# Kernel optimization log

Hardware: AMD Instinct MI355X
Metric: run time of the kernel (lower is better)

The kernel has to match this reference:

```python
import jax, jax.numpy as jnp
import numpy as np

NODES = 8192
RANK = 10  # hardcoded inner dim in the original module


def setup_inputs() -> dict:
    key = jax.random.key(0)
    k1, k2 = jax.random.split(key)
    nodevec1 = jax.random.normal(k1, (NODES, RANK), dtype=jnp.float32)
    nodevec2 = jax.random.normal(k2, (RANK, NODES), dtype=jnp.float32)
    return {"nodevec1": nodevec1, "nodevec2": nodevec2}


def reference(nodevec1, nodevec2):
    # [N, 10] @ [10, N] -> [N, N]; relu; row softmax (dim=1)
    scores = jax.nn.relu(jnp.matmul(nodevec1, nodevec2))
    return jax.nn.softmax(scores, axis=1)
```

## Files before the change

kernel.cpp:

```cpp
#include <hip/hip_runtime.h>


#define NODES 8192
#define RANK  10

#define K1_TPB   1024
#define K1_NWAVE (K1_TPB / 64)
#define K1_RPB   32
#define K1_NBLK  (NODES / K1_RPB)
#define K1_CHUNK 8

__global__ __launch_bounds__(K1_TPB)
void rowsum_kernel(const float* __restrict__ nv1,
                   const float* __restrict__ nv2,
                   float* __restrict__ rowinv)
{
    const int t    = threadIdx.x;
    const int lane = t & 63;
    const int wave = t >> 6;
    const int row0 = blockIdx.x * K1_RPB;

    float4 b[2][RANK];
#pragma unroll
    for (int g = 0; g < 2; ++g) {
        const int j = g * 4096 + t * 4;
#pragma unroll
        for (int k = 0; k < RANK; ++k)
            b[g][k] = *reinterpret_cast<const float4*>(nv2 + k * NODES + j);
    }

    __shared__ float red[K1_NWAVE][K1_RPB];

    for (int c = 0; c < K1_RPB; c += K1_CHUNK) {
        float psum[K1_CHUNK];
#pragma unroll
        for (int r = 0; r < K1_CHUNK; ++r) {
            const int row = row0 + c + r;
            float a[RANK];
#pragma unroll
            for (int k = 0; k < RANK; ++k) a[k] = nv1[row * RANK + k];

            float sum = 0.0f;
#pragma unroll
            for (int g = 0; g < 2; ++g) {
                float4 acc = make_float4(0.f, 0.f, 0.f, 0.f);
#pragma unroll
                for (int k = 0; k < RANK; ++k) {
                    acc.x = fmaf(a[k], b[g][k].x, acc.x);
                    acc.y = fmaf(a[k], b[g][k].y, acc.y);
                    acc.z = fmaf(a[k], b[g][k].z, acc.z);
                    acc.w = fmaf(a[k], b[g][k].w, acc.w);
                }
                sum += __expf(fmaxf(acc.x, 0.f)) + __expf(fmaxf(acc.y, 0.f))
                     + __expf(fmaxf(acc.z, 0.f)) + __expf(fmaxf(acc.w, 0.f));
            }
            psum[r] = sum;
        }
#pragma unroll
        for (int r = 0; r < K1_CHUNK; ++r) {
#pragma unroll
            for (int m = 32; m >= 1; m >>= 1)
                psum[r] += __shfl_xor(psum[r], m, 64);
        }
        if (lane == 0) {
#pragma unroll
            for (int r = 0; r < K1_CHUNK; ++r) red[wave][c + r] = psum[r];
        }
    }

    __syncthreads();
    if (t < K1_RPB) {
        float s = 0.0f;
#pragma unroll
        for (int w = 0; w < K1_NWAVE; ++w) s += red[w][t];
        rowinv[row0 + t] = 1.0f / s;
    }
}

#define K2_TPB  256
#define K2_RPB  8
#define K2_SEGS (NODES / (K2_TPB * 4))
#define K2_NBLK ((NODES / K2_RPB) * K2_SEGS)

__global__ __launch_bounds__(K2_TPB, 8)
void stream_kernel(const float* __restrict__ nv1,
                   const float* __restrict__ nv2,
                   const float* __restrict__ rowinv,
                   float* __restrict__ out)
{
    const int t      = threadIdx.x;
    const int seg    = blockIdx.x & (K2_SEGS - 1);
    const int rowblk = blockIdx.x >> 3;
    const int row0   = rowblk * K2_RPB;
    const int j      = seg * (K2_TPB * 4) + t * 4;

    float4 b[RANK];
#pragma unroll
    for (int k = 0; k < RANK; ++k)
        b[k] = *reinterpret_cast<const float4*>(nv2 + k * NODES + j);

#pragma unroll 2
    for (int r = 0; r < K2_RPB; ++r) {
        const int row = row0 + r;
        const float inv = rowinv[row];
        float a[RANK];
#pragma unroll
        for (int k = 0; k < RANK; ++k) a[k] = nv1[row * RANK + k];

        float4 acc = make_float4(0.f, 0.f, 0.f, 0.f);
#pragma unroll
        for (int k = 0; k < RANK; ++k) {
            acc.x = fmaf(a[k], b[k].x, acc.x);
            acc.y = fmaf(a[k], b[k].y, acc.y);
            acc.z = fmaf(a[k], b[k].z, acc.z);
            acc.w = fmaf(a[k], b[k].w, acc.w);
        }
        float4 o;
        o.x = __expf(fmaxf(acc.x, 0.f)) * inv;
        o.y = __expf(fmaxf(acc.y, 0.f)) * inv;
        o.z = __expf(fmaxf(acc.z, 0.f)) * inv;
        o.w = __expf(fmaxf(acc.w, 0.f)) * inv;
        *reinterpret_cast<float4*>(out + (size_t)row * NODES + j) = o;
    }
}

extern "C" void kernel_launch(void* const* d_in, const int* in_sizes, int n_in,
                              void* d_out, int out_size, void* d_ws, size_t ws_size,
                              hipStream_t stream)
{
    const float* nv1 = (const float*)d_in[0];
    const float* nv2 = (const float*)d_in[1];
    float* out    = (float*)d_out;
    float* rowinv = (float*)d_ws;

    rowsum_kernel<<<K1_NBLK, K1_TPB, 0, stream>>>(nv1, nv2, rowinv);
    stream_kernel<<<K2_NBLK, K2_TPB, 0, stream>>>(nv1, nv2, rowinv, out);
}
```

Before: 288.1 us.

## Fold log2e into B, use exp2 with log-sum offset, persistent stream grid

```diff
diff --git a/kernel.cpp b/kernel.cpp
--- a/kernel.cpp
+++ b/kernel.cpp
@@ -3,6 +3,7 @@
 
 #define NODES 8192
 #define RANK  10
+#define L2E   1.4426950408889634f
 
 #define K1_TPB   1024
 #define K1_NWAVE (K1_TPB / 64)
@@ -13,7 +14,7 @@
 __global__ __launch_bounds__(K1_TPB)
 void rowsum_kernel(const float* __restrict__ nv1,
                    const float* __restrict__ nv2,
-                   float* __restrict__ rowinv)
+                   float* __restrict__ rowsum)
 {
     const int t    = threadIdx.x;
     const int lane = t & 63;
@@ -25,8 +26,11 @@
     for (int g = 0; g < 2; ++g) {
         const int j = g * 4096 + t * 4;
 #pragma unroll
-        for (int k = 0; k < RANK; ++k)
-            b[g][k] = *reinterpret_cast<const float4*>(nv2 + k * NODES + j);
+        for (int k = 0; k < RANK; ++k) {
+            float4 v = *reinterpret_cast<const float4*>(nv2 + k * NODES + j);
+            v.x *= L2E; v.y *= L2E; v.z *= L2E; v.w *= L2E;
+            b[g][k] = v;
+        }
     }
 
     __shared__ float red[K1_NWAVE][K1_RPB];
@@ -51,8 +55,10 @@
                     acc.z = fmaf(a[k], b[g][k].z, acc.z);
                     acc.w = fmaf(a[k], b[g][k].w, acc.w);
                 }
-                sum += __expf(fmaxf(acc.x, 0.f)) + __expf(fmaxf(acc.y, 0.f))
-                     + __expf(fmaxf(acc.z, 0.f)) + __expf(fmaxf(acc.w, 0.f));
+                sum += __builtin_amdgcn_exp2f(fmaxf(acc.x, 0.f))
+                     + __builtin_amdgcn_exp2f(fmaxf(acc.y, 0.f))
+                     + __builtin_amdgcn_exp2f(fmaxf(acc.z, 0.f))
+                     + __builtin_amdgcn_exp2f(fmaxf(acc.w, 0.f));
             }
             psum[r] = sum;
         }
@@ -73,54 +79,62 @@
         float s = 0.0f;
 #pragma unroll
         for (int w = 0; w < K1_NWAVE; ++w) s += red[w][t];
-        rowinv[row0 + t] = 1.0f / s;
+        rowsum[row0 + t] = s;
     }
 }
 
-#define K2_TPB  256
-#define K2_RPB  8
-#define K2_SEGS (NODES / (K2_TPB * 4))
-#define K2_NBLK ((NODES / K2_RPB) * K2_SEGS)
+#define K2_TPB   256
+#define K2_RPB   8
+#define K2_SEGW  (K2_TPB * 4)
+#define K2_NSEG  (NODES / K2_SEGW)
+#define K2_GRID  2048
+#define K2_RSTR  (K2_GRID / K2_NSEG)
+#define K2_ITERS (NODES / K2_RPB / K2_RSTR)
 
 __global__ __launch_bounds__(K2_TPB, 8)
 void stream_kernel(const float* __restrict__ nv1,
                    const float* __restrict__ nv2,
-                   const float* __restrict__ rowinv,
+                   const float* __restrict__ rowsum,
                    float* __restrict__ out)
 {
-    const int t      = threadIdx.x;
-    const int seg    = blockIdx.x & (K2_SEGS - 1);
-    const int rowblk = blockIdx.x >> 3;
-    const int row0   = rowblk * K2_RPB;
-    const int j      = seg * (K2_TPB * 4) + t * 4;
+    const int t     = threadIdx.x;
+    const int seg   = blockIdx.x & (K2_NSEG - 1);
+    const int rbase = blockIdx.x >> 3;
+    const int j     = seg * K2_SEGW + t * 4;
 
     float4 b[RANK];
 #pragma unroll
-    for (int k = 0; k < RANK; ++k)
-        b[k] = *reinterpret_cast<const float4*>(nv2 + k * NODES + j);
+    for (int k = 0; k < RANK; ++k) {
+        float4 v = *reinterpret_cast<const float4*>(nv2 + k * NODES + j);
+        v.x *= L2E; v.y *= L2E; v.z *= L2E; v.w *= L2E;
+        b[k] = v;
+    }
 
+    for (int i = 0; i < K2_ITERS; ++i) {
+        const int row0 = (rbase + i * K2_RSTR) * K2_RPB;
 #pragma unroll 2
-    for (int r = 0; r < K2_RPB; ++r) {
-        const int row = row0 + r;
-        const float inv = rowinv[row];
-        float a[RANK];
+        for (int r = 0; r < K2_RPB; ++r) {
+            const int row = row0 + r;
+            const float nc = -__builtin_amdgcn_logf(rowsum[row]);
+            float a[RANK];
 #pragma unroll
-        for (int k = 0; k < RANK; ++k) a[k] = nv1[row * RANK + k];
+            for (int k = 0; k < RANK; ++k) a[k] = nv1[row * RANK + k];
 
-        float4 acc = make_float4(0.f, 0.f, 0.f, 0.f);
+            float4 acc = make_float4(0.f, 0.f, 0.f, 0.f);
 #pragma unroll
-        for (int k = 0; k < RANK; ++k) {
-            acc.x = fmaf(a[k], b[k].x, acc.x);
-            acc.y = fmaf(a[k], b[k].y, acc.y);
-            acc.z = fmaf(a[k], b[k].z, acc.z);
-            acc.w = fmaf(a[k], b[k].w, acc.w);
+            for (int k = 0; k < RANK; ++k) {
+                acc.x = fmaf(a[k], b[k].x, acc.x);
+                acc.y = fmaf(a[k], b[k].y, acc.y);
+                acc.z = fmaf(a[k], b[k].z, acc.z);
+                acc.w = fmaf(a[k], b[k].w, acc.w);
+            }
+            float4 o;
+            o.x = __builtin_amdgcn_exp2f(fmaxf(acc.x, 0.f) + nc);
+            o.y = __builtin_amdgcn_exp2f(fmaxf(acc.y, 0.f) + nc);
+            o.z = __builtin_amdgcn_exp2f(fmaxf(acc.z, 0.f) + nc);
+            o.w = __builtin_amdgcn_exp2f(fmaxf(acc.w, 0.f) + nc);
+            *reinterpret_cast<float4*>(out + (size_t)row * NODES + j) = o;
         }
-        float4 o;
-        o.x = __expf(fmaxf(acc.x, 0.f)) * inv;
-        o.y = __expf(fmaxf(acc.y, 0.f)) * inv;
-        o.z = __expf(fmaxf(acc.z, 0.f)) * inv;
-        o.w = __expf(fmaxf(acc.w, 0.f)) * inv;
-        *reinterpret_cast<float4*>(out + (size_t)row * NODES + j) = o;
     }
 }
 
@@ -131,8 +145,8 @@
     const float* nv1 = (const float*)d_in[0];
     const float* nv2 = (const float*)d_in[1];
     float* out    = (float*)d_out;
-    float* rowinv = (float*)d_ws;
+    float* rowsum = (float*)d_ws;
 
-    rowsum_kernel<<<K1_NBLK, K1_TPB, 0, stream>>>(nv1, nv2, rowinv);
-    stream_kernel<<<K2_NBLK, K2_TPB, 0, stream>>>(nv1, nv2, rowinv, out);
+    rowsum_kernel<<<K1_NBLK, K1_TPB, 0, stream>>>(nv1, nv2, rowsum);
+    stream_kernel<<<K2_GRID, K2_TPB, 0, stream>>>(nv1, nv2, rowsum, out);
 }
```

Measured after the change: 289.7 us, median of 2. Within noise of the previous version (+0.5%).
